# Kernel tuning notes

Hardware: AMD Instinct MI355X
Metric: run time of the kernel (lower is better)

## Reference

```python
import jax, jax.numpy as jnp
import numpy as np

N_NODES = 50000
N_EDGES = 800000
IN_FEATS = 128
H_FEATS = 128
OUT_FEATS = 64


def _mean_agg(h, src, dst, n_nodes):
    # mean over in-neighbors: sum h[src] into dst, divide by in-degree (0 for isolated nodes)
    summed = jax.ops.segment_sum(h[src], dst, num_segments=n_nodes)  # [N, d]
    deg = jax.ops.segment_sum(jnp.ones((src.shape[0],), h.dtype), dst, num_segments=n_nodes)
    return summed / jnp.maximum(deg, 1.0)[:, None]


def setup_inputs() -> dict:
    key = jax.random.key(0)
    ks = jax.random.split(key, 10)
    s = 0.05
    return {
        "inputs": jax.random.normal(ks[0], (N_NODES, IN_FEATS), jnp.float32),
        "fc_W": jax.random.normal(ks[1], (H_FEATS, IN_FEATS), jnp.float32) * s,
        "fc_b": jax.random.normal(ks[2], (H_FEATS,), jnp.float32) * s,
        "W": jax.random.normal(ks[3], (3, H_FEATS, H_FEATS), jnp.float32) * s,
        "b": jax.random.normal(ks[4], (3, H_FEATS), jnp.float32) * s,
        "W_last": jax.random.normal(ks[5], (OUT_FEATS, H_FEATS), jnp.float32) * s,
        "b_last": jax.random.normal(ks[6], (OUT_FEATS,), jnp.float32) * s,
        "eps": jnp.zeros((4,), jnp.float32),
        "src": jax.random.randint(ks[7], (N_EDGES,), 0, N_NODES, jnp.int32),
        "dst": jax.random.randint(ks[8], (N_EDGES,), 0, N_NODES, jnp.int32),
    }


def reference(inputs, fc_W, fc_b, W, b, W_last, b_last, eps, src, dst):
    n = inputs.shape[0]
    # input SLP
    h = jax.nn.relu(inputs @ fc_W.T + fc_b)
    # 3 hidden GIN layers: relu(Linear((1+eps)*h + mean_agg(h)))  (dropout = eval identity)
    for i in range(3):
        agg = _mean_agg(h, src, dst, n)
        h = jax.nn.relu(((1.0 + eps[i]) * h + agg) @ W[i].T + b[i])
    # last GIN layer (no ReLU)
    agg = _mean_agg(h, src, dst, n)
    h = ((1.0 + eps[3]) * h + agg) @ W_last.T + b_last
    return h
```

## Files before the change

kernel.cpp:

```cpp
#include <hip/hip_runtime.h>

#define N_NODES 50000
#define N_EDGES 800000
#define GRP 8
#define NPG (N_NODES / GRP)
#define EPB 8192
#define NSTRIPE ((N_EDGES + EPB - 1) / EPB)

typedef __attribute__((ext_vector_type(8))) short short8;
typedef __attribute__((ext_vector_type(4))) float float4v;

__device__ inline unsigned short f2bf(float f) {
    unsigned u = __float_as_uint(f);
    unsigned r = u + 0x7fff + ((u >> 16) & 1);
    return (unsigned short)(r >> 16);
}
__device__ inline float bf2f(unsigned short h) {
    return __uint_as_float(((unsigned)h) << 16);
}


__global__ void scan_partial(const int* __restrict__ deg, int* __restrict__ partial) {
    __shared__ int sm[256];
    int t = threadIdx.x;
    int i = blockIdx.x * 256 + t;
    sm[t] = (i < N_NODES) ? deg[i] : 0;
    __syncthreads();
    for (int o = 128; o > 0; o >>= 1) {
        if (t < o) sm[t] += sm[t + o];
        __syncthreads();
    }
    if (t == 0) partial[blockIdx.x] = sm[0];
}

__global__ void scan_offsets(int* __restrict__ partial, int* __restrict__ row_ptr, int nparts) {
    __shared__ int sm[256];
    int t = threadIdx.x;
    int v = (t < nparts) ? partial[t] : 0;
    sm[t] = v;
    __syncthreads();
    for (int o = 1; o < 256; o <<= 1) {
        int x = sm[t];
        int a = (t >= o) ? sm[t - o] : 0;
        __syncthreads();
        sm[t] = x + a;
        __syncthreads();
    }
    if (t < nparts) partial[t] = sm[t] - v;
    if (t == nparts - 1) row_ptr[N_NODES] = sm[t];
}

__global__ void scan_final(const int* __restrict__ deg, const int* __restrict__ partial,
                           int* __restrict__ row_ptr, int* __restrict__ fill_pos) {
    __shared__ int sm[256];
    int t = threadIdx.x;
    int i = blockIdx.x * 256 + t;
    int v = (i < N_NODES) ? deg[i] : 0;
    sm[t] = v;
    __syncthreads();
    for (int o = 1; o < 256; o <<= 1) {
        int x = sm[t];
        int a = (t >= o) ? sm[t - o] : 0;
        __syncthreads();
        sm[t] = x + a;
        __syncthreads();
    }
    if (i < N_NODES) {
        int ex = sm[t] - v + partial[blockIdx.x];
        row_ptr[i] = ex;
        fill_pos[i] = ex;
    }
}


__global__ void __launch_bounds__(256) fused_hist_prep(
    const int* __restrict__ dst, int* __restrict__ deg, const float* __restrict__ fcW,
    const float* __restrict__ W, const float* __restrict__ Wl, unsigned short* __restrict__ hi,
    unsigned short* __restrict__ lo) {
    int bx = blockIdx.x;
    if (bx < GRP * NSTRIPE) {
        int g = bx & 7;
        int stripe = bx >> 3;
        int nlo = g * NPG, nhi = nlo + NPG;
        int base = stripe * EPB + threadIdx.x;
#pragma unroll 4
        for (int k = 0; k < EPB / 256; k++) {
            int i = base + k * 256;
            if (i < N_EDGES) {
                int d = dst[i];
                if (d >= nlo && d < nhi) atomicAdd(&deg[d], 1);
            }
        }
    } else {
        int i = (bx - GRP * NSTRIPE) * 256 + threadIdx.x;
        float v;
        if (i < 16384) v = fcW[i];
        else if (i < 65536) v = W[i - 16384];
        else if (i < 73728) v = Wl[i - 65536];
        else return;
        unsigned short h = f2bf(v);
        hi[i] = h;
        lo[i] = f2bf(v - bf2f(h));
    }
}


template <int COLS, bool RELU, bool WRITE_BF>
__device__ __forceinline__ void gemm_body(int bx, const float* __restrict__ U,
                                          const unsigned short* __restrict__ Whi,
                                          const unsigned short* __restrict__ Wlo,
                                          const float* __restrict__ bias, float* __restrict__ out,
                                          unsigned short* __restrict__ outbf, int nrows) {
    int wave = threadIdx.x >> 6;
    int lane = threadIdx.x & 63;
    int m = lane & 15;
    int quad = lane >> 4;
    int r0 = bx * 64 + wave * 16;
    int rowA = r0 + m;
    if (rowA >= nrows) rowA = nrows - 1;

    short8 ahi[4], alo[4];
    const float* arow = U + (size_t)rowA * 128 + quad * 8;
#pragma unroll
    for (int kc = 0; kc < 4; kc++) {
        float4 f0 = *(const float4*)(arow + kc * 32);
        float4 f1 = *(const float4*)(arow + kc * 32 + 4);
        float fv[8] = {f0.x, f0.y, f0.z, f0.w, f1.x, f1.y, f1.z, f1.w};
#pragma unroll
        for (int j = 0; j < 8; j++) {
            unsigned short h = f2bf(fv[j]);
            ahi[kc][j] = (short)h;
            alo[kc][j] = (short)f2bf(fv[j] - bf2f(h));
        }
    }

#pragma unroll
    for (int nt = 0; nt < COLS / 16; nt++) {
        int n = nt * 16 + m;
        const unsigned short* bhp = Whi + (size_t)n * 128 + quad * 8;
        const unsigned short* blp = Wlo + (size_t)n * 128 + quad * 8;
        float4v acc = {0.f, 0.f, 0.f, 0.f};
#pragma unroll
        for (int kc = 0; kc < 4; kc++) {
            short8 bh = *(const short8*)(bhp + kc * 32);
            short8 bl = *(const short8*)(blp + kc * 32);
            acc = __builtin_amdgcn_mfma_f32_16x16x32_bf16(ahi[kc], bh, acc, 0, 0, 0);
            acc = __builtin_amdgcn_mfma_f32_16x16x32_bf16(alo[kc], bh, acc, 0, 0, 0);
            acc = __builtin_amdgcn_mfma_f32_16x16x32_bf16(ahi[kc], bl, acc, 0, 0, 0);
        }
        float bv = bias[n];
#pragma unroll
        for (int i = 0; i < 4; i++) {
            int r = r0 + quad * 4 + i;
            if (r < nrows) {
                float v = acc[i] + bv;
                if (RELU) v = fmaxf(v, 0.f);
                out[(size_t)r * COLS + n] = v;
                if (WRITE_BF) outbf[(size_t)r * COLS + n] = f2bf(v);
            }
        }
    }
}

template <int COLS, bool RELU, bool WRITE_BF>
__global__ void __launch_bounds__(256) gemm_mfma(const float* __restrict__ U,
                                                 const unsigned short* __restrict__ Whi,
                                                 const unsigned short* __restrict__ Wlo,
                                                 const float* __restrict__ bias,
                                                 float* __restrict__ out,
                                                 unsigned short* __restrict__ outbf, int nrows) {
    gemm_body<COLS, RELU, WRITE_BF>(blockIdx.x, U, Whi, Wlo, bias, out, outbf, nrows);
}


__global__ void __launch_bounds__(256) fused_fill_gemm(
    const int* __restrict__ src, const int* __restrict__ dst, int* __restrict__ fill_pos,
    int* __restrict__ esrc, const float* __restrict__ X, const unsigned short* __restrict__ whi,
    const unsigned short* __restrict__ wlo, const float* __restrict__ fcb, float* __restrict__ h,
    unsigned short* __restrict__ hbf) {
    int bx = blockIdx.x;
    if (bx < GRP * NSTRIPE) {
        int g = bx & 7;
        int stripe = bx >> 3;
        int nlo = g * NPG, nhi = nlo + NPG;
        int base = stripe * EPB + threadIdx.x;
#pragma unroll 4
        for (int k = 0; k < EPB / 256; k++) {
            int i = base + k * 256;
            if (i < N_EDGES) {
                int d = dst[i];
                if (d >= nlo && d < nhi) {
                    int p = atomicAdd(&fill_pos[d], 1);
                    esrc[p] = src[i];
                }
            }
        }
    } else {
        gemm_body<128, true, true>(bx - GRP * NSTRIPE, X, whi, wlo, fcb, h, hbf, N_NODES);
    }
}


__global__ void agg_kernel(const float* __restrict__ h, const unsigned short* __restrict__ hbf,
                           const int* __restrict__ row_ptr, const int* __restrict__ esrc,
                           const float* __restrict__ eps, int layer, float* __restrict__ u) {
    int gtid = blockIdx.x * 256 + threadIdx.x;
    int node = gtid >> 6;
    int lane = threadIdx.x & 63;
    if (node >= N_NODES) return;
    node = __builtin_amdgcn_readfirstlane(node);
    int beg = __builtin_amdgcn_readfirstlane(row_ptr[node]);
    int end = __builtin_amdgcn_readfirstlane(row_ptr[node + 1]);

    const unsigned short* hl = hbf + lane * 2;
    float a0x = 0.f, a0y = 0.f, a1x = 0.f, a1y = 0.f;
    float a2x = 0.f, a2y = 0.f, a3x = 0.f, a3y = 0.f;
    int e = beg;
    for (; e + 3 < end; e += 4) {
        int s0 = esrc[e], s1 = esrc[e + 1], s2 = esrc[e + 2], s3 = esrc[e + 3];
        unsigned v0 = *(const unsigned*)(hl + (size_t)s0 * 128);
        unsigned v1 = *(const unsigned*)(hl + (size_t)s1 * 128);
        unsigned v2 = *(const unsigned*)(hl + (size_t)s2 * 128);
        unsigned v3 = *(const unsigned*)(hl + (size_t)s3 * 128);
        a0x += bf2f((unsigned short)v0); a0y += bf2f((unsigned short)(v0 >> 16));
        a1x += bf2f((unsigned short)v1); a1y += bf2f((unsigned short)(v1 >> 16));
        a2x += bf2f((unsigned short)v2); a2y += bf2f((unsigned short)(v2 >> 16));
        a3x += bf2f((unsigned short)v3); a3y += bf2f((unsigned short)(v3 >> 16));
    }
    for (; e < end; e++) {
        int s = esrc[e];
        unsigned v = *(const unsigned*)(hl + (size_t)s * 128);
        a0x += bf2f((unsigned short)v);
        a0y += bf2f((unsigned short)(v >> 16));
    }
    float sx = (a0x + a1x) + (a2x + a3x);
    float sy = (a0y + a1y) + (a2y + a3y);
    int d = end - beg;
    float inv = (d > 0) ? 1.0f / (float)d : 0.0f;
    float ep = 1.0f + eps[layer];
    float2 hv = *(const float2*)(h + (size_t)node * 128 + lane * 2);
    float2 r;
    r.x = ep * hv.x + sx * inv;
    r.y = ep * hv.y + sy * inv;
    *(float2*)(u + (size_t)node * 128 + lane * 2) = r;
}


extern "C" void kernel_launch(void* const* d_in, const int* in_sizes, int n_in,
                              void* d_out, int out_size, void* d_ws, size_t ws_size,
                              hipStream_t stream) {
    const float* X   = (const float*)d_in[0];
    const float* fcW = (const float*)d_in[1];
    const float* fcb = (const float*)d_in[2];
    const float* W   = (const float*)d_in[3];
    const float* b   = (const float*)d_in[4];
    const float* Wl  = (const float*)d_in[5];
    const float* bl  = (const float*)d_in[6];
    const float* eps = (const float*)d_in[7];
    const int* src   = (const int*)d_in[8];
    const int* dst   = (const int*)d_in[9];
    float* out = (float*)d_out;

    float* h = (float*)d_ws;
    float* u = h + (size_t)N_NODES * 128;
    unsigned short* hbf = (unsigned short*)(u + (size_t)N_NODES * 128);
    unsigned short* whi = hbf + (size_t)N_NODES * 128;
    unsigned short* wlo = whi + 73728;
    int* deg      = (int*)(wlo + 73728);
    int* row_ptr  = deg + N_NODES;
    int* fill_pos = row_ptr + (N_NODES + 1);
    int* partial  = fill_pos + N_NODES;
    int* esrc     = partial + 256;

    const int NB = (N_NODES + 255) / 256;
    const int gemm_blocks = (N_NODES + 63) / 64;
    const int agg_blocks = (N_NODES * 64 + 255) / 256;
    const int hist_blocks = GRP * NSTRIPE;
    const int prep_blocks = (73728 + 255) / 256;

    hipMemsetAsync(deg, 0, N_NODES * sizeof(int), stream);
    fused_hist_prep<<<hist_blocks + prep_blocks, 256, 0, stream>>>(dst, deg, fcW, W, Wl, whi, wlo);
    scan_partial<<<NB, 256, 0, stream>>>(deg, partial);
    scan_offsets<<<1, 256, 0, stream>>>(partial, row_ptr, NB);
    scan_final<<<NB, 256, 0, stream>>>(deg, partial, row_ptr, fill_pos);

    fused_fill_gemm<<<hist_blocks + gemm_blocks, 256, 0, stream>>>(src, dst, fill_pos, esrc, X,
                                                                   whi, wlo, fcb, h, hbf);

    for (int i = 0; i < 3; i++) {
        agg_kernel<<<agg_blocks, 256, 0, stream>>>(h, hbf, row_ptr, esrc, eps, i, u);
        gemm_mfma<128, true, true><<<gemm_blocks, 256, 0, stream>>>(
            u, whi + 16384 + (size_t)i * 16384, wlo + 16384 + (size_t)i * 16384,
            b + (size_t)i * 128, h, hbf, N_NODES);
    }

    agg_kernel<<<agg_blocks, 256, 0, stream>>>(h, hbf, row_ptr, esrc, eps, 3, u);
    gemm_mfma<64, false, false><<<gemm_blocks, 256, 0, stream>>>(u, whi + 65536, wlo + 65536, bl,
                                                                 out, nullptr, N_NODES);
}
```

Baseline: 452.0 us.

## Replace per-node atomic CSR build with two-pass bucketed counting sort

Result: faster. 429.7 us (-4.9%).

```diff
diff --git a/kernel.cpp b/kernel.cpp
--- a/kernel.cpp
+++ b/kernel.cpp
@@ -2,8 +2,7 @@
 
 #define N_NODES 50000
 #define N_EDGES 800000
-#define GRP 8
-#define NPG (N_NODES / GRP)
+#define NBUCK 196
 #define EPB 8192
 #define NSTRIPE ((N_EDGES + EPB - 1) / EPB)
 
@@ -20,79 +19,26 @@
 }
 
 
-__global__ void scan_partial(const int* __restrict__ deg, int* __restrict__ partial) {
-    __shared__ int sm[256];
-    int t = threadIdx.x;
-    int i = blockIdx.x * 256 + t;
-    sm[t] = (i < N_NODES) ? deg[i] : 0;
-    __syncthreads();
-    for (int o = 128; o > 0; o >>= 1) {
-        if (t < o) sm[t] += sm[t + o];
-        __syncthreads();
-    }
-    if (t == 0) partial[blockIdx.x] = sm[0];
-}
-
-__global__ void scan_offsets(int* __restrict__ partial, int* __restrict__ row_ptr, int nparts) {
-    __shared__ int sm[256];
-    int t = threadIdx.x;
-    int v = (t < nparts) ? partial[t] : 0;
-    sm[t] = v;
-    __syncthreads();
-    for (int o = 1; o < 256; o <<= 1) {
-        int x = sm[t];
-        int a = (t >= o) ? sm[t - o] : 0;
-        __syncthreads();
-        sm[t] = x + a;
-        __syncthreads();
-    }
-    if (t < nparts) partial[t] = sm[t] - v;
-    if (t == nparts - 1) row_ptr[N_NODES] = sm[t];
-}
-
-__global__ void scan_final(const int* __restrict__ deg, const int* __restrict__ partial,
-                           int* __restrict__ row_ptr, int* __restrict__ fill_pos) {
-    __shared__ int sm[256];
-    int t = threadIdx.x;
-    int i = blockIdx.x * 256 + t;
-    int v = (i < N_NODES) ? deg[i] : 0;
-    sm[t] = v;
-    __syncthreads();
-    for (int o = 1; o < 256; o <<= 1) {
-        int x = sm[t];
-        int a = (t >= o) ? sm[t - o] : 0;
-        __syncthreads();
-        sm[t] = x + a;
-        __syncthreads();
-    }
-    if (i < N_NODES) {
-        int ex = sm[t] - v + partial[blockIdx.x];
-        row_ptr[i] = ex;
-        fill_pos[i] = ex;
-    }
-}
-
-
 __global__ void __launch_bounds__(256) fused_hist_prep(
-    const int* __restrict__ dst, int* __restrict__ deg, const float* __restrict__ fcW,
+    const int* __restrict__ dst, int* __restrict__ bcnt, const float* __restrict__ fcW,
     const float* __restrict__ W, const float* __restrict__ Wl, unsigned short* __restrict__ hi,
     unsigned short* __restrict__ lo) {
     int bx = blockIdx.x;
-    if (bx < GRP * NSTRIPE) {
-        int g = bx & 7;
-        int stripe = bx >> 3;
-        int nlo = g * NPG, nhi = nlo + NPG;
-        int base = stripe * EPB + threadIdx.x;
+    if (bx < NSTRIPE) {
+        __shared__ int lhist[256];
+        int t = threadIdx.x;
+        lhist[t] = 0;
+        __syncthreads();
+        int base = bx * EPB + t;
 #pragma unroll 4
         for (int k = 0; k < EPB / 256; k++) {
             int i = base + k * 256;
-            if (i < N_EDGES) {
-                int d = dst[i];
-                if (d >= nlo && d < nhi) atomicAdd(&deg[d], 1);
-            }
-        }
+            if (i < N_EDGES) atomicAdd(&lhist[((unsigned)dst[i]) >> 8], 1);
+        }
+        __syncthreads();
+        if (t < NBUCK) atomicAdd(&bcnt[t], lhist[t]);
     } else {
-        int i = (bx - GRP * NSTRIPE) * 256 + threadIdx.x;
+        int i = (bx - NSTRIPE) * 256 + threadIdx.x;
         float v;
         if (i < 16384) v = fcW[i];
         else if (i < 65536) v = W[i - 16384];
@@ -101,6 +47,31 @@
         unsigned short h = f2bf(v);
         hi[i] = h;
         lo[i] = f2bf(v - bf2f(h));
+    }
+}
+
+
+__global__ void bucket_scan(const int* __restrict__ bcnt, int* __restrict__ boff,
+                            int* __restrict__ cursor, int* __restrict__ row_ptr) {
+    __shared__ int sm[256];
+    int t = threadIdx.x;
+    int v = (t < NBUCK) ? bcnt[t] : 0;
+    sm[t] = v;
+    __syncthreads();
+    for (int o = 1; o < 256; o <<= 1) {
+        int x = sm[t];
+        int a = (t >= o) ? sm[t - o] : 0;
+        __syncthreads();
+        sm[t] = x + a;
+        __syncthreads();
+    }
+    if (t < NBUCK) {
+        boff[t] = sm[t] - v;
+        cursor[t] = sm[t] - v;
+    }
+    if (t == NBUCK - 1) {
+        boff[NBUCK] = sm[t];
+        row_ptr[N_NODES] = sm[t];
     }
 }
 
@@ -173,30 +144,78 @@
 }
 
 
-__global__ void __launch_bounds__(256) fused_fill_gemm(
-    const int* __restrict__ src, const int* __restrict__ dst, int* __restrict__ fill_pos,
-    int* __restrict__ esrc, const float* __restrict__ X, const unsigned short* __restrict__ whi,
+__global__ void __launch_bounds__(256) fused_binA_gemm(
+    const int* __restrict__ src, const int* __restrict__ dst, int* __restrict__ cursor,
+    int* __restrict__ packed, const float* __restrict__ X, const unsigned short* __restrict__ whi,
     const unsigned short* __restrict__ wlo, const float* __restrict__ fcb, float* __restrict__ h,
     unsigned short* __restrict__ hbf) {
     int bx = blockIdx.x;
-    if (bx < GRP * NSTRIPE) {
-        int g = bx & 7;
-        int stripe = bx >> 3;
-        int nlo = g * NPG, nhi = nlo + NPG;
-        int base = stripe * EPB + threadIdx.x;
+    if (bx < NSTRIPE) {
+        __shared__ int lcount[256];
+        __shared__ int lbase[256];
+        int t = threadIdx.x;
+        lcount[t] = 0;
+        __syncthreads();
+        int base = bx * EPB + t;
+#pragma unroll 4
+        for (int k = 0; k < EPB / 256; k++) {
+            int i = base + k * 256;
+            if (i < N_EDGES) atomicAdd(&lcount[((unsigned)dst[i]) >> 8], 1);
+        }
+        __syncthreads();
+        if (t < NBUCK) {
+            lbase[t] = atomicAdd(&cursor[t], lcount[t]);
+            lcount[t] = 0;
+        }
+        __syncthreads();
 #pragma unroll 4
         for (int k = 0; k < EPB / 256; k++) {
             int i = base + k * 256;
             if (i < N_EDGES) {
                 int d = dst[i];
-                if (d >= nlo && d < nhi) {
-                    int p = atomicAdd(&fill_pos[d], 1);
-                    esrc[p] = src[i];
-                }
+                int wb = ((unsigned)d) >> 8;
+                int p = lbase[wb] + atomicAdd(&lcount[wb], 1);
+                packed[p] = ((d & 255) << 16) | src[i];
             }
         }
     } else {
-        gemm_body<128, true, true>(bx - GRP * NSTRIPE, X, whi, wlo, fcb, h, hbf, N_NODES);
+        gemm_body<128, true, true>(bx - NSTRIPE, X, whi, wlo, fcb, h, hbf, N_NODES);
+    }
+}
+
+
+__global__ void __launch_bounds__(256) binB_kernel(const int* __restrict__ packed,
+                                                   const int* __restrict__ boff,
+                                                   int* __restrict__ row_ptr,
+                                                   int* __restrict__ esrc) {
+    __shared__ int sm[256];
+    __shared__ int curs[256];
+    int b = blockIdx.x;
+    int t = threadIdx.x;
+    int e0 = boff[b], e1 = boff[b + 1];
+    curs[t] = 0;
+    __syncthreads();
+    for (int i = e0 + t; i < e1; i += 256) atomicAdd(&curs[((unsigned)packed[i]) >> 16], 1);
+    __syncthreads();
+    int v = curs[t];
+    sm[t] = v;
+    __syncthreads();
+    for (int o = 1; o < 256; o <<= 1) {
+        int x = sm[t];
+        int a = (t >= o) ? sm[t - o] : 0;
+        __syncthreads();
+        sm[t] = x + a;
+        __syncthreads();
+    }
+    int excl = sm[t] - v;
+    curs[t] = excl;
+    int node = b * 256 + t;
+    if (node < N_NODES) row_ptr[node] = e0 + excl;
+    __syncthreads();
+    for (int i = e0 + t; i < e1; i += 256) {
+        unsigned w = (unsigned)packed[i];
+        int p = atomicAdd(&curs[w >> 16], 1);
+        esrc[e0 + p] = (int)(w & 0xFFFFu);
     }
 }
 
@@ -266,26 +285,23 @@
     unsigned short* hbf = (unsigned short*)(u + (size_t)N_NODES * 128);
     unsigned short* whi = hbf + (size_t)N_NODES * 128;
     unsigned short* wlo = whi + 73728;
-    int* deg      = (int*)(wlo + 73728);
-    int* row_ptr  = deg + N_NODES;
-    int* fill_pos = row_ptr + (N_NODES + 1);
-    int* partial  = fill_pos + N_NODES;
-    int* esrc     = partial + 256;
-
-    const int NB = (N_NODES + 255) / 256;
+    int* bcnt    = (int*)(wlo + 73728);
+    int* boff    = bcnt + NBUCK;
+    int* cursor  = boff + NBUCK + 1;
+    int* row_ptr = cursor + NBUCK;
+    int* packed  = row_ptr + N_NODES + 1;
+    int* esrc    = packed + N_EDGES;
+
     const int gemm_blocks = (N_NODES + 63) / 64;
     const int agg_blocks = (N_NODES * 64 + 255) / 256;
-    const int hist_blocks = GRP * NSTRIPE;
     const int prep_blocks = (73728 + 255) / 256;
 
-    hipMemsetAsync(deg, 0, N_NODES * sizeof(int), stream);
-    fused_hist_prep<<<hist_blocks + prep_blocks, 256, 0, stream>>>(dst, deg, fcW, W, Wl, whi, wlo);
-    scan_partial<<<NB, 256, 0, stream>>>(deg, partial);
-    scan_offsets<<<1, 256, 0, stream>>>(partial, row_ptr, NB);
-    scan_final<<<NB, 256, 0, stream>>>(deg, partial, row_ptr, fill_pos);
-
-    fused_fill_gemm<<<hist_blocks + gemm_blocks, 256, 0, stream>>>(src, dst, fill_pos, esrc, X,
-                                                                   whi, wlo, fcb, h, hbf);
+    hipMemsetAsync(bcnt, 0, NBUCK * sizeof(int), stream);
+    fused_hist_prep<<<NSTRIPE + prep_blocks, 256, 0, stream>>>(dst, bcnt, fcW, W, Wl, whi, wlo);
+    bucket_scan<<<1, 256, 0, stream>>>(bcnt, boff, cursor, row_ptr);
+    fused_binA_gemm<<<NSTRIPE + gemm_blocks, 256, 0, stream>>>(src, dst, cursor, packed, X, whi,
+                                                               wlo, fcb, h, hbf);
+    binB_kernel<<<NBUCK, 256, 0, stream>>>(packed, boff, row_ptr, esrc);
 
     for (int i = 0; i < 3; i++) {
         agg_kernel<<<agg_blocks, 256, 0, stream>>>(h, hbf, row_ptr, esrc, eps, i, u);
```
